# Performance work log

Measured on AMD Instinct MI355X. Metric: run time of the kernel, lower is better.

## Reference

```python
import jax, jax.numpy as jnp
import numpy as np

B, S, I, H, O = 256, 2048, 32, 128, 1


def setup_inputs() -> dict:
    key = jax.random.key(0)
    ks = jax.random.split(key, 9)
    sI = 1.0 / np.sqrt(I)
    sH = 1.0 / np.sqrt(H)
    sD = 1.0 / np.sqrt(H * S)
    return {
        "x": jax.random.normal(ks[0], (B, S, I), jnp.float32),
        "Wi": jax.random.normal(ks[1], (I, H), jnp.float32) * sI,
        "bi": jax.random.normal(ks[2], (H,), jnp.float32) * sI,
        "Wh": jax.random.normal(ks[3], (H, H), jnp.float32) * sH,
        "bh": jax.random.normal(ks[4], (H,), jnp.float32) * sH,
        "Wa": jax.random.normal(ks[5], (H, 1), jnp.float32) * sH,
        "ba": jax.random.normal(ks[6], (1,), jnp.float32) * sH,
        "Wd": jax.random.normal(ks[7], (H * S, O), jnp.float32) * sD,
        "bd": jax.random.normal(ks[8], (O,), jnp.float32) * sD,
        "resDepth": 4,
    }


def _branch_ids(seq_len: int, resDepth: int) -> np.ndarray:
    # Encodes the per-step branch of ResRNN_Cell.forward (static in i, resDepth):
    # 0: i==0 (set hstart, h0 stays zero)   1: i==lag-2 -> h0=tanh(hn+hstart)
    # 4: resDepth==1 -> h0=tanh(hn+h0)      2: i%resDepth==0 -> h0=tanh(hn+ht), ht=hn
    # 3: else -> h0=tanh(hn)
    br = np.full(seq_len, 3, dtype=np.int32)
    br[(np.arange(seq_len) % resDepth) == 0] = 2
    if resDepth == 1:
        br[:] = 4
    br[seq_len - 2] = 1
    br[0] = 0
    return br


def reference(x, Wi, bi, Wh, bh, Wa, ba, Wd, bd, resDepth):
    batch, seq_len, _ = x.shape
    hid = Wh.shape[0]
    br = _branch_ids(seq_len, int(resDepth))
    f0, f1, f2, f4 = (jnp.asarray(br == k) for k in (0, 1, 2, 4))
    xs = jnp.swapaxes(x, 0, 1)  # (S, B, I)
    z = jnp.zeros((batch, hid), x.dtype)

    def step(carry, inp):
        h0, ht, hstart = carry
        xt, g0, g1, g2, g4 = inp
        hn = xt @ Wi + bi + h0 @ Wh + bh  # (B, H)
        hstart = jnp.where(g0, hn, hstart)
        cand = jnp.where(g1, jnp.tanh(hn + hstart),
               jnp.where(g4, jnp.tanh(hn + h0),
               jnp.where(g2, jnp.tanh(hn + ht), jnp.tanh(hn))))
        h0n = jnp.where(g0, h0, cand)  # at i==0 h0 is NOT updated in the original
        htn = jnp.where(g2, hn, ht)
        return (h0n, htn, hstart), hn

    _, hiddens = jax.lax.scan(step, (z, z, z), (xs, f0, f1, f2, f4))
    # hiddens: (S, B, H) == torch.cat(outputs, 0)
    scores = hiddens @ Wa + ba  # (S, B, 1)
    # faithful to the original's .view((batchSize, -1)) on (S,B,1)-contiguous data
    att = jax.nn.softmax(scores.reshape(batch, seq_len), axis=-1)
    att = att.reshape(seq_len, batch, 1)
    weighted = hiddens * att  # (S, B, H)
    # faithful to .view(-1, hiddenNum * seq_len) on (S,B,H)-contiguous data
    flat = weighted.reshape(batch, seq_len * hid)
    return flat @ Wd + bd
```

## Files before the change

### kernel.cpp

```cpp
#include <hip/hip_runtime.h>
#include <math.h>

#define B_ 256
#define S_ 2048
#define I_ 32
#define H_ 128

__device__ __forceinline__ void sync_lds() {
    asm volatile("" ::: "memory");
    asm volatile("s_waitcnt lgkmcnt(0)" ::: "memory");
    __builtin_amdgcn_s_barrier();
    asm volatile("" ::: "memory");
}

__device__ __forceinline__ float fast_tanh(float z) {
    float e = __expf(2.0f * z);
    return 1.0f - 2.0f / (e + 1.0f);
}

template <int CTRL>
__device__ __forceinline__ float dppf(float v) {
    return __int_as_float(__builtin_amdgcn_update_dpp(
        0, __float_as_int(v), CTRL, 0xF, 0xF, false));
}

__device__ __forceinline__ float swz_xor16(float v) {
    return __int_as_float(__builtin_amdgcn_ds_swizzle(__float_as_int(v), 0x401F));
}
__device__ __forceinline__ float bperm_f(int addr_bytes, float v) {
    return __int_as_float(__builtin_amdgcn_ds_bpermute(addr_bytes, __float_as_int(v)));
}

#define MAC1(hval, idx)                              \
    a0 = fmaf(hval, WhR[(idx) * 2 + 0], a0);         \
    a1 = fmaf(hval, WhR[(idx) * 2 + 1], a1);
#define MAC4(hv, j)                                  \
    MAC1((hv).x, 4 * (j) + 0)                        \
    MAC1((hv).y, 4 * (j) + 1)                        \
    MAC1((hv).z, 4 * (j) + 2)                        \
    MAC1((hv).w, 4 * (j) + 3)

#define STEP_BODY(g, PH, XA, XB, CPH)                                         \
  {                                                                           \
    const int s_ = (g) * 8 + (PH);                                            \
    const float4* hsrc = (const float4*)&h0_lds[(PH) & 1][0];                 \
    float4 hv0 = hsrc[kg];                                                    \
    float4 hv1 = hsrc[kg + 8];                                                \
    float4 hv2 = hsrc[kg + 16];                                               \
    float4 hv3 = hsrc[kg + 24];                                               \
    if (s_ >= 1) {                \
      float r = uP;                                                           \
      r += dppf<0xB1>(r);                                                     \
      r += dppf<0x124>(r);                                                    \
      r += swz_xor16(r);                                                      \
      r += bperm_f(bp32, r);                                                  \
      if ((l & 0x3D) == 0)                                                    \
        ((float*)&pl_lds[(unsigned)(s_ - 1) & 3][w])[(l >> 1) & 1] = r;       \
    }                                                                         \
    if (w == 0 && s_ >= 2) {                \
      float2 pp = pl_lds[(unsigned)(s_ - 2) & 3][l & 7];                      \
      float px = pp.x, py = pp.y;                                             \
      px += dppf<0xB1>(px);  py += dppf<0xB1>(py);                            \
      px += dppf<0x4E>(px);  py += dppf<0x4E>(py);                            \
      px += dppf<0x124>(px); py += dppf<0x124>(py);                           \
      if (l == 0) part[((s_ - 2) << 8) + b] = make_float2(px, py);            \
    }                                                                         \
    float a0 = 0.f, a1 = 0.f;                                                 \
    MAC4(hv0, 0) MAC4(hv1, 1) MAC4(hv2, 2) MAC4(hv3, 3)                       \
    a0 += dppf<0xB1>(a0);                                                     \
    a1 += dppf<0xB1>(a1);                                                     \
    float t = kb0b ? a1 : a0;                                                 \
    float xwp = biasR;                                                        \
    xwp = fmaf((XA).x, WiC[0], xwp);                                          \
    xwp = fmaf((XA).y, WiC[1], xwp);                                          \
    xwp = fmaf((XA).z, WiC[2], xwp);                                          \
    xwp = fmaf((XA).w, WiC[3], xwp);                                          \
    xwp = fmaf((XB).x, WiC[4], xwp);                                          \
    xwp = fmaf((XB).y, WiC[5], xwp);                                          \
    xwp = fmaf((XB).z, WiC[6], xwp);                                          \
    xwp = fmaf((XB).w, WiC[7], xwp);                                          \
    t += xwp;                                \
    t += dppf<0x4E>(t);                                                       \
    t += dppf<0x128>(t);                                                      \
    float hn = t;                                                             \
    if (s_ < S_ - 2) {           \
      const float4* xr = (const float4*)(xgrp + ((PH) + 2) * I_);             \
      (XA) = xr[0]; (XB) = xr[1];                                             \
    }                                                                         \
    uP = hn * (CPH);                         \
    float h0n;                                                                \
    if (s_ == 0)            { hstartR = hn; h0n = 0.0f; }                     \
    else if (s_ == S_ - 2)  { h0n = fast_tanh(hn + hstartR); }                \
    else if (rd == 1)       { h0n = fast_tanh(hn + h0R); }                    \
    else if (cnt == 0)      { h0n = fast_tanh(hn + htR); htR = hn; }          \
    else                    { h0n = fast_tanh(hn); }                          \
    h0R = h0n;                                                                \
    if (wmask) h0_lds[((PH) + 1) & 1][hf] = h0n;                              \
    cnt = (cnt + 1 == rd) ? 0 : cnt + 1;                                      \
    sync_lds();                                                               \
  }

__global__ __launch_bounds__(512)
__attribute__((amdgpu_waves_per_eu(2, 2)))
void rnn_kernel(
    const float* __restrict__ x, const float* __restrict__ Wi,
    const float* __restrict__ bi, const float* __restrict__ Wh,
    const float* __restrict__ bh, const float* __restrict__ Wa,
    const float* __restrict__ Wd, const int* __restrict__ rdp,
    float2* __restrict__ part)
{
    const int b = blockIdx.x;
    const int t = threadIdx.x;
    const int w = t >> 6;
    const int l = t & 63;
    const int  kg    = (l & 3) | (((l >> 3) & 1) << 2);
    const int  hg    = ((l >> 2) & 1) | (((l >> 4) & 1) << 1)
                     | (((l >> 5) & 1) << 2);
    const int  hbase = 16 * w + 2 * hg;
    const int  hf    = hbase + (l & 1);
    const bool kb0b  = (l & 1);
    const bool wmask = ((l & 0xA) == 0);
    const int  i0x   = 8 * (((l >> 1) & 1) | (((l >> 3) & 1) << 1));
    const int  bp32  = (l ^ 32) << 2;

    __shared__ __align__(16) float h0_lds[2][H_];
    __shared__ __align__(8)  float2 pl_lds[4][8];

    const int rd = rdp[0];
    if (t < H_) h0_lds[0][t] = 0.0f;

    float WhR[32];
#pragma unroll
    for (int j = 0; j < 4; ++j)
#pragma unroll
        for (int c = 0; c < 4; ++c) {
            int k = 4 * kg + 32 * j + c;
            float2 wv = *(const float2*)(Wh + (size_t)k * H_ + hbase);
            WhR[(4 * j + c) * 2 + 0] = wv.x;
            WhR[(4 * j + c) * 2 + 1] = wv.y;
        }
    float WiC[8];
#pragma unroll
    for (int i = 0; i < 8; ++i) WiC[i] = Wi[(size_t)(i0x + i) * H_ + hf];
    const float biasR = wmask ? (bi[hf] + bh[hf]) : 0.0f;

    const bool clsq = (l >> 1) & 1;
    const float waC = Wa[hf];
    float cph[8];
#pragma unroll
    for (int K = 0; K < 8; ++K)
        cph[K] = clsq ? Wd[(K << 15) + (b << 7) + hf] : waC;

    const float* xgrp = x + (size_t)b * (S_ * I_) + i0x;
    float4 xA0 = ((const float4*)xgrp)[0];
    float4 xB0 = ((const float4*)xgrp)[1];
    float4 xA1 = ((const float4*)(xgrp + I_))[0];
    float4 xB1 = ((const float4*)(xgrp + I_))[1];

    sync_lds();

    float htR = 0.f, hstartR = 0.f, h0R = 0.f;
    float uP = 0.f;
    int cnt = 0;

    for (int g = 0; g < S_ / 8; ++g) {
        STEP_BODY(g, 0, xA0, xB0, cph[0])
        STEP_BODY(g, 1, xA1, xB1, cph[1])
        STEP_BODY(g, 2, xA0, xB0, cph[2])
        STEP_BODY(g, 3, xA1, xB1, cph[3])
        STEP_BODY(g, 4, xA0, xB0, cph[4])
        STEP_BODY(g, 5, xA1, xB1, cph[5])
        STEP_BODY(g, 6, xA0, xB0, cph[6])
        STEP_BODY(g, 7, xA1, xB1, cph[7])
        xgrp += 8 * I_;
    }

    {
        float r = uP;
        r += dppf<0xB1>(r);
        r += dppf<0x124>(r);
        r += swz_xor16(r);
        r += bperm_f(bp32, r);
        if ((l & 0x3D) == 0)
            ((float*)&pl_lds[3][w])[(l >> 1) & 1] = r;
    }
    sync_lds();
    if (w == 0) {
#pragma unroll
        for (int e = 0; e < 2; ++e) {
            float2 pp = pl_lds[2 + e][l & 7];
            float px = pp.x, py = pp.y;
            px += dppf<0xB1>(px);  py += dppf<0xB1>(py);
            px += dppf<0x4E>(px);  py += dppf<0x4E>(py);
            px += dppf<0x124>(px); py += dppf<0x124>(py);
            if (l == 0) part[((S_ - 2 + e) << 8) + b] = make_float2(px, py);
        }
    }
}

__global__ __launch_bounds__(256) void attn_kernel(
    const float2* __restrict__ part, const float* __restrict__ bd,
    float* __restrict__ out)
{
    const int r = blockIdx.x;
    const int t = threadIdx.x;
    float sc[8], dv[8];
    float mx = -1e30f;
#pragma unroll
    for (int u = 0; u < 8; ++u) {
        int f = (r << 11) + (u << 8) + t;
        float2 a = part[f];
        sc[u] = a.x;
        dv[u] = a.y;
        mx = fmaxf(mx, sc[u]);
    }
    __shared__ float redm[4], redz[4], redw[4];
#pragma unroll
    for (int off = 32; off > 0; off >>= 1) mx = fmaxf(mx, __shfl_xor(mx, off, 64));
    if ((t & 63) == 0) redm[t >> 6] = mx;
    __syncthreads();
    mx = fmaxf(fmaxf(redm[0], redm[1]), fmaxf(redm[2], redm[3]));
    float z = 0.f, wv = 0.f;
#pragma unroll
    for (int u = 0; u < 8; ++u) {
        float e = __expf(sc[u] - mx);
        z += e;
        wv += e * dv[u];
    }
#pragma unroll
    for (int off = 32; off > 0; off >>= 1) {
        z += __shfl_xor(z, off, 64);
        wv += __shfl_xor(wv, off, 64);
    }
    if ((t & 63) == 0) { redz[t >> 6] = z; redw[t >> 6] = wv; }
    __syncthreads();
    if (t == 0) {
        float Z = redz[0] + redz[1] + redz[2] + redz[3];
        float W = redw[0] + redw[1] + redw[2] + redw[3];
        out[r] = bd[0] + W / Z;
    }
}

extern "C" void kernel_launch(void* const* d_in, const int* in_sizes, int n_in,
                              void* d_out, int out_size, void* d_ws, size_t ws_size,
                              hipStream_t stream) {
    const float* x  = (const float*)d_in[0];
    const float* Wi = (const float*)d_in[1];
    const float* bi = (const float*)d_in[2];
    const float* Wh = (const float*)d_in[3];
    const float* bh = (const float*)d_in[4];
    const float* Wa = (const float*)d_in[5];
    const float* Wd = (const float*)d_in[7];
    const float* bd = (const float*)d_in[8];
    const int*  rdp = (const int*)d_in[9];

    float2* part = (float2*)d_ws;

    rnn_kernel<<<B_, 512, 0, stream>>>(x, Wi, bi, Wh, bh, Wa, Wd, rdp, part);
    attn_kernel<<<B_, 256, 0, stream>>>(part, bd, (float*)d_out);
}
```

Baseline: 1.035 ms.

## Halve RNN block to 4 waves with 4 hidden columns per lane

Each RNN block now runs with 256 threads instead of 512. Every lane holds four hidden columns of Wh and Wi as float4 registers, and the input projection is folded into the same accumulators before the cross-lane reduction. Using fewer waves per batch row should cut barrier cost and the cross-wave reduction work on each serial timestep. The trade-off is more FMAs per lane and a longer dependent chain in every step, and the per-lane register footprint roughly doubles.

```diff
diff --git a/kernel.cpp b/kernel.cpp
--- a/kernel.cpp
+++ b/kernel.cpp
@@ -31,61 +31,66 @@
     return __int_as_float(__builtin_amdgcn_ds_bpermute(addr_bytes, __float_as_int(v)));
 }
 
-#define MAC1(hval, idx)                              \
-    a0 = fmaf(hval, WhR[(idx) * 2 + 0], a0);         \
-    a1 = fmaf(hval, WhR[(idx) * 2 + 1], a1);
-#define MAC4(hv, j)                                  \
-    MAC1((hv).x, 4 * (j) + 0)                        \
-    MAC1((hv).y, 4 * (j) + 1)                        \
-    MAC1((hv).z, 4 * (j) + 2)                        \
-    MAC1((hv).w, 4 * (j) + 3)
-
-#define STEP_BODY(g, PH, XA, XB, CPH)                                         \
+#define MACC(hval, idx)                              \
+    a0 = fmaf(hval, WhR4[(idx)].x, a0);              \
+    a1 = fmaf(hval, WhR4[(idx)].y, a1);              \
+    a2 = fmaf(hval, WhR4[(idx)].z, a2);              \
+    a3 = fmaf(hval, WhR4[(idx)].w, a3);
+#define MACQ(hv, q)                                  \
+    MACC((hv).x, 4 * (q) + 0)                        \
+    MACC((hv).y, 4 * (q) + 1)                        \
+    MACC((hv).z, 4 * (q) + 2)                        \
+    MACC((hv).w, 4 * (q) + 3)
+
+#define STEP_BODY(g, PH, XS, CPH)                                             \
   {                                                                           \
     const int s_ = (g) * 8 + (PH);                                            \
     const float4* hsrc = (const float4*)&h0_lds[(PH) & 1][0];                 \
-    float4 hv0 = hsrc[kg];                                                    \
-    float4 hv1 = hsrc[kg + 8];                                                \
-    float4 hv2 = hsrc[kg + 16];                                               \
-    float4 hv3 = hsrc[kg + 24];                                               \
+    float4 hv0 = hsrc[kg3];                                                   \
+    float4 hv1 = hsrc[kg3 + 8];                                               \
+    float4 hv2 = hsrc[kg3 + 16];                                              \
+    float4 hv3 = hsrc[kg3 + 24];                                              \
     if (s_ >= 1) {                \
       float r = uP;                                                           \
       r += dppf<0xB1>(r);                                                     \
-      r += dppf<0x124>(r);                                                    \
+      r += dppf<0x4E>(r);                                                     \
+      r += dppf<0x141>(r);                                                    \
       r += swz_xor16(r);                                                      \
       r += bperm_f(bp32, r);                                                  \
-      if ((l & 0x3D) == 0)                                                    \
-        ((float*)&pl_lds[(unsigned)(s_ - 1) & 3][w])[(l >> 1) & 1] = r;       \
+      if ((l & 0x37) == 0)                                                    \
+        ((float*)&pl_lds[(unsigned)(s_ - 1) & 3][w])[(l >> 3) & 1] = r;       \
     }                                                                         \
     if (w == 0 && s_ >= 2) {                \
-      float2 pp = pl_lds[(unsigned)(s_ - 2) & 3][l & 7];                      \
+      float2 pp = pl_lds[(unsigned)(s_ - 2) & 3][l & 3];                      \
       float px = pp.x, py = pp.y;                                             \
       px += dppf<0xB1>(px);  py += dppf<0xB1>(py);                            \
       px += dppf<0x4E>(px);  py += dppf<0x4E>(py);                            \
-      px += dppf<0x124>(px); py += dppf<0x124>(py);                           \
       if (l == 0) part[((s_ - 2) << 8) + b] = make_float2(px, py);            \
     }                                                                         \
-    float a0 = 0.f, a1 = 0.f;                                                 \
-    MAC4(hv0, 0) MAC4(hv1, 1) MAC4(hv2, 2) MAC4(hv3, 3)                       \
-    a0 += dppf<0xB1>(a0);                                                     \
-    a1 += dppf<0xB1>(a1);                                                     \
-    float t = kb0b ? a1 : a0;                                                 \
-    float xwp = biasR;                                                        \
-    xwp = fmaf((XA).x, WiC[0], xwp);                                          \
-    xwp = fmaf((XA).y, WiC[1], xwp);                                          \
-    xwp = fmaf((XA).z, WiC[2], xwp);                                          \
-    xwp = fmaf((XA).w, WiC[3], xwp);                                          \
-    xwp = fmaf((XB).x, WiC[4], xwp);                                          \
-    xwp = fmaf((XB).y, WiC[5], xwp);                                          \
-    xwp = fmaf((XB).z, WiC[6], xwp);                                          \
-    xwp = fmaf((XB).w, WiC[7], xwp);                                          \
-    t += xwp;                                \
-    t += dppf<0x4E>(t);                                                       \
-    t += dppf<0x128>(t);                                                      \
-    float hn = t;                                                             \
+    float a0 = (XS).x * WiC4[0].x;                                            \
+    float a1 = (XS).x * WiC4[0].y;                                            \
+    float a2 = (XS).x * WiC4[0].z;                                            \
+    float a3 = (XS).x * WiC4[0].w;                                            \
+    a0 = fmaf((XS).y, WiC4[1].x, a0); a1 = fmaf((XS).y, WiC4[1].y, a1);       \
+    a2 = fmaf((XS).y, WiC4[1].z, a2); a3 = fmaf((XS).y, WiC4[1].w, a3);       \
+    a0 = fmaf((XS).z, WiC4[2].x, a0); a1 = fmaf((XS).z, WiC4[2].y, a1);       \
+    a2 = fmaf((XS).z, WiC4[2].z, a2); a3 = fmaf((XS).z, WiC4[2].w, a3);       \
+    a0 = fmaf((XS).w, WiC4[3].x, a0); a1 = fmaf((XS).w, WiC4[3].y, a1);       \
+    a2 = fmaf((XS).w, WiC4[3].z, a2); a3 = fmaf((XS).w, WiC4[3].w, a3);       \
+    MACQ(hv0, 0) MACQ(hv1, 1) MACQ(hv2, 2) MACQ(hv3, 3)                       \
+    float s0 = a0 + dppf<0xB1>(a0);                                           \
+    float s1 = a1 + dppf<0xB1>(a1);                                           \
+    float s2 = a2 + dppf<0xB1>(a2);                                           \
+    float s3 = a3 + dppf<0xB1>(a3);                                           \
+    float u0 = kb0 ? s1 : s0;                                                 \
+    float u1 = kb0 ? s3 : s2;                                                 \
+    u0 += dppf<0x4E>(u0);                                                     \
+    u1 += dppf<0x4E>(u1);                                                     \
+    float tt = kb1 ? u1 : u0;                                                 \
+    tt += dppf<0x128>(tt);                                                    \
+    float hn = tt + biasR;                                                    \
     if (s_ < S_ - 2) {           \
-      const float4* xr = (const float4*)(xgrp + ((PH) + 2) * I_);             \
-      (XA) = xr[0]; (XB) = xr[1];                                             \
+      (XS) = *(const float4*)(xgrp + ((PH) + 2) * I_);                        \
     }                                                                         \
     uP = hn * (CPH);                         \
     float h0n;                                                                \
@@ -100,8 +105,8 @@
     sync_lds();                                                               \
   }
 
-__global__ __launch_bounds__(512)
-__attribute__((amdgpu_waves_per_eu(2, 2)))
+__global__ __launch_bounds__(256)
+__attribute__((amdgpu_waves_per_eu(1, 1)))
 void rnn_kernel(
     const float* __restrict__ x, const float* __restrict__ Wi,
     const float* __restrict__ bi, const float* __restrict__ Wh,
@@ -113,38 +118,38 @@
     const int t = threadIdx.x;
     const int w = t >> 6;
     const int l = t & 63;
-    const int  kg    = (l & 3) | (((l >> 3) & 1) << 2);
+    const int  kg3   = (l & 3) | (((l >> 3) & 1) << 2);
     const int  hg    = ((l >> 2) & 1) | (((l >> 4) & 1) << 1)
                      | (((l >> 5) & 1) << 2);
-    const int  hbase = 16 * w + 2 * hg;
-    const int  hf    = hbase + (l & 1);
-    const bool kb0b  = (l & 1);
-    const bool wmask = ((l & 0xA) == 0);
-    const int  i0x   = 8 * (((l >> 1) & 1) | (((l >> 3) & 1) << 1));
-    const int  bp32  = (l ^ 32) << 2;
+    const int  hbase4 = 32 * w + 4 * hg;
+    const int  hf     = hbase4 + (l & 3);
+    const bool kb0    = (l & 1);
+    const bool kb1    = (l >> 1) & 1;
+    const bool wmask  = ((l & 8) == 0);
+    const int  i0x    = 4 * kg3;
+    const int  bp32   = (l ^ 32) << 2;
 
     __shared__ __align__(16) float h0_lds[2][H_];
-    __shared__ __align__(8)  float2 pl_lds[4][8];
+    __shared__ __align__(8)  float2 pl_lds[4][4];
 
     const int rd = rdp[0];
     if (t < H_) h0_lds[0][t] = 0.0f;
 
-    float WhR[32];
-#pragma unroll
-    for (int j = 0; j < 4; ++j)
+    float4 WhR4[16];
+#pragma unroll
+    for (int q = 0; q < 4; ++q)
 #pragma unroll
         for (int c = 0; c < 4; ++c) {
-            int k = 4 * kg + 32 * j + c;
-            float2 wv = *(const float2*)(Wh + (size_t)k * H_ + hbase);
-            WhR[(4 * j + c) * 2 + 0] = wv.x;
-            WhR[(4 * j + c) * 2 + 1] = wv.y;
+            int k = 4 * (kg3 + 8 * q) + c;
+            WhR4[q * 4 + c] = *(const float4*)(Wh + (size_t)k * H_ + hbase4);
         }
-    float WiC[8];
-#pragma unroll
-    for (int i = 0; i < 8; ++i) WiC[i] = Wi[(size_t)(i0x + i) * H_ + hf];
-    const float biasR = wmask ? (bi[hf] + bh[hf]) : 0.0f;
-
-    const bool clsq = (l >> 1) & 1;
+    float4 WiC4[4];
+#pragma unroll
+    for (int i = 0; i < 4; ++i)
+        WiC4[i] = *(const float4*)(Wi + (size_t)(i0x + i) * H_ + hbase4);
+    const float biasR = bi[hf] + bh[hf];
+
+    const bool clsq = (l >> 3) & 1;
     const float waC = Wa[hf];
     float cph[8];
 #pragma unroll
@@ -152,10 +157,8 @@
         cph[K] = clsq ? Wd[(K << 15) + (b << 7) + hf] : waC;
 
     const float* xgrp = x + (size_t)b * (S_ * I_) + i0x;
-    float4 xA0 = ((const float4*)xgrp)[0];
-    float4 xB0 = ((const float4*)xgrp)[1];
-    float4 xA1 = ((const float4*)(xgrp + I_))[0];
-    float4 xB1 = ((const float4*)(xgrp + I_))[1];
+    float4 xS0 = *(const float4*)xgrp;
+    float4 xS1 = *(const float4*)(xgrp + I_);
 
     sync_lds();
 
@@ -164,35 +167,35 @@
     int cnt = 0;
 
     for (int g = 0; g < S_ / 8; ++g) {
-        STEP_BODY(g, 0, xA0, xB0, cph[0])
-        STEP_BODY(g, 1, xA1, xB1, cph[1])
-        STEP_BODY(g, 2, xA0, xB0, cph[2])
-        STEP_BODY(g, 3, xA1, xB1, cph[3])
-        STEP_BODY(g, 4, xA0, xB0, cph[4])
-        STEP_BODY(g, 5, xA1, xB1, cph[5])
-        STEP_BODY(g, 6, xA0, xB0, cph[6])
-        STEP_BODY(g, 7, xA1, xB1, cph[7])
+        STEP_BODY(g, 0, xS0, cph[0])
+        STEP_BODY(g, 1, xS1, cph[1])
+        STEP_BODY(g, 2, xS0, cph[2])
+        STEP_BODY(g, 3, xS1, cph[3])
+        STEP_BODY(g, 4, xS0, cph[4])
+        STEP_BODY(g, 5, xS1, cph[5])
+        STEP_BODY(g, 6, xS0, cph[6])
+        STEP_BODY(g, 7, xS1, cph[7])
         xgrp += 8 * I_;
     }
 
     {
         float r = uP;
         r += dppf<0xB1>(r);
-        r += dppf<0x124>(r);
+        r += dppf<0x4E>(r);
+        r += dppf<0x141>(r);
         r += swz_xor16(r);
         r += bperm_f(bp32, r);
-        if ((l & 0x3D) == 0)
-            ((float*)&pl_lds[3][w])[(l >> 1) & 1] = r;
+        if ((l & 0x37) == 0)
+            ((float*)&pl_lds[3][w])[(l >> 3) & 1] = r;
     }
     sync_lds();
     if (w == 0) {
 #pragma unroll
         for (int e = 0; e < 2; ++e) {
-            float2 pp = pl_lds[2 + e][l & 7];
+            float2 pp = pl_lds[2 + e][l & 3];
             float px = pp.x, py = pp.y;
             px += dppf<0xB1>(px);  py += dppf<0xB1>(py);
             px += dppf<0x4E>(px);  py += dppf<0x4E>(py);
-            px += dppf<0x124>(px); py += dppf<0x124>(py);
             if (l == 0) part[((S_ - 2 + e) << 8) + b] = make_float2(px, py);
         }
     }
@@ -256,6 +259,6 @@
 
     float2* part = (float2*)d_ws;
 
-    rnn_kernel<<<B_, 512, 0, stream>>>(x, Wi, bi, Wh, bh, Wa, Wd, rdp, part);
+    rnn_kernel<<<B_, 256, 0, stream>>>(x, Wi, bi, Wh, bh, Wa, Wd, rdp, part);
     attn_kernel<<<B_, 256, 0, stream>>>(part, bd, (float*)d_out);
 }
```

Measured after the change: 1.079 ms. 1.04x slower.

## Peel first/last step groups, lighten per-step reductions and rotate combine across waves

Applied to the files above, without the earlier changes.

Peels the first and last 8-step groups so the middle loop runs a branch-light step with a select-based residual instead of the if-chain. The per-step attention/dense partial reduction drops the cross-half swizzle and bpermute, writing 32 partials per ring slot to LDS instead of 8. The final combine, which now does more DPP work plus a swizzle, rotates across waves by step phase instead of always running on wave 0. This shortens the serial critical path of each recurrent step at the cost of a larger LDS ring and more code.

```diff
diff --git a/kernel.cpp b/kernel.cpp
--- a/kernel.cpp
+++ b/kernel.cpp
@@ -26,9 +26,6 @@
 
 __device__ __forceinline__ float swz_xor16(float v) {
     return __int_as_float(__builtin_amdgcn_ds_swizzle(__float_as_int(v), 0x401F));
-}
-__device__ __forceinline__ float bperm_f(int addr_bytes, float v) {
-    return __int_as_float(__builtin_amdgcn_ds_bpermute(addr_bytes, __float_as_int(v)));
 }
 
 #define MAC1(hval, idx)                              \
@@ -40,36 +37,33 @@
     MAC1((hv).z, 4 * (j) + 2)                        \
     MAC1((hv).w, 4 * (j) + 3)
 
-#define STEP_BODY(g, PH, XA, XB, CPH)                                         \
-  {                                                                           \
-    const int s_ = (g) * 8 + (PH);                                            \
-    const float4* hsrc = (const float4*)&h0_lds[(PH) & 1][0];                 \
-    float4 hv0 = hsrc[kg];                                                    \
-    float4 hv1 = hsrc[kg + 8];                                                \
-    float4 hv2 = hsrc[kg + 16];                                               \
-    float4 hv3 = hsrc[kg + 24];                                               \
-    if (s_ >= 1) {                \
+#define UP_REDUCE(RING)                                                       \
+    {                                                                         \
       float r = uP;                                                           \
       r += dppf<0xB1>(r);                                                     \
       r += dppf<0x124>(r);                                                    \
-      r += swz_xor16(r);                                                      \
-      r += bperm_f(bp32, r);                                                  \
-      if ((l & 0x3D) == 0)                                                    \
-        ((float*)&pl_lds[(unsigned)(s_ - 1) & 3][w])[(l >> 1) & 1] = r;       \
-    }                                                                         \
-    if (w == 0 && s_ >= 2) {                \
-      float2 pp = pl_lds[(unsigned)(s_ - 2) & 3][l & 7];                      \
+      if ((l & 0xD) == 0)                                                     \
+        ((float*)&pl_lds[RING][(w << 2) | ((l >> 4) & 3)])[(l >> 1) & 1] = r; \
+    }
+
+#define PL_COMBINE(RING, SIDX)                                                \
+    {                                                                         \
+      float2 pp = pl_lds[RING][l & 31];                                       \
       float px = pp.x, py = pp.y;                                             \
       px += dppf<0xB1>(px);  py += dppf<0xB1>(py);                            \
       px += dppf<0x4E>(px);  py += dppf<0x4E>(py);                            \
-      px += dppf<0x124>(px); py += dppf<0x124>(py);                           \
-      if (l == 0) part[((s_ - 2) << 8) + b] = make_float2(px, py);            \
-    }                                                                         \
+      px += dppf<0x141>(px); py += dppf<0x141>(py);                           \
+      px += dppf<0x128>(px); py += dppf<0x128>(py);                           \
+      px += swz_xor16(px);   py += swz_xor16(py);                             \
+      if (l == 0) part[((SIDX) << 8) + b] = make_float2(px, py);              \
+    }
+
+#define MAT_CORE(XA, XB)                                                      \
     float a0 = 0.f, a1 = 0.f;                                                 \
     MAC4(hv0, 0) MAC4(hv1, 1) MAC4(hv2, 2) MAC4(hv3, 3)                       \
     a0 += dppf<0xB1>(a0);                                                     \
     a1 += dppf<0xB1>(a1);                                                     \
-    float t = kb0b ? a1 : a0;                                                 \
+    float tt = kb0b ? a1 : a0;                                                \
     float xwp = biasR;                                                        \
     xwp = fmaf((XA).x, WiC[0], xwp);                                          \
     xwp = fmaf((XA).y, WiC[1], xwp);                                          \
@@ -79,21 +73,59 @@
     xwp = fmaf((XB).y, WiC[5], xwp);                                          \
     xwp = fmaf((XB).z, WiC[6], xwp);                                          \
     xwp = fmaf((XB).w, WiC[7], xwp);                                          \
-    t += xwp;                                \
-    t += dppf<0x4E>(t);                                                       \
-    t += dppf<0x128>(t);                                                      \
-    float hn = t;                                                             \
-    if (s_ < S_ - 2) {           \
+    tt += xwp;                                                                \
+    tt += dppf<0x4E>(tt);                                                     \
+    tt += dppf<0x128>(tt);                                                    \
+    const float hn = tt;
+
+#define STEP_FULL(g, PH, XA, XB, CPH)                                         \
+  {                                                                           \
+    const int s_ = (g) * 8 + (PH);                                            \
+    const float4* hsrc = (const float4*)&h0_lds[(PH) & 1][0];                 \
+    float4 hv0 = hsrc[kg];                                                    \
+    float4 hv1 = hsrc[kg + 8];                                                \
+    float4 hv2 = hsrc[kg + 16];                                               \
+    float4 hv3 = hsrc[kg + 24];                                               \
+    if (s_ >= 1) UP_REDUCE(((PH) + 3) & 3)                                    \
+    if (w == (PH) && s_ >= 2) PL_COMBINE(((PH) + 2) & 3, s_ - 2)              \
+    MAT_CORE(XA, XB)                                                          \
+    if (s_ < S_ - 2) {                                                        \
       const float4* xr = (const float4*)(xgrp + ((PH) + 2) * I_);             \
       (XA) = xr[0]; (XB) = xr[1];                                             \
     }                                                                         \
-    uP = hn * (CPH);                         \
+    uP = hn * (CPH);                                                          \
     float h0n;                                                                \
     if (s_ == 0)            { hstartR = hn; h0n = 0.0f; }                     \
     else if (s_ == S_ - 2)  { h0n = fast_tanh(hn + hstartR); }                \
     else if (rd == 1)       { h0n = fast_tanh(hn + h0R); }                    \
     else if (cnt == 0)      { h0n = fast_tanh(hn + htR); htR = hn; }          \
     else                    { h0n = fast_tanh(hn); }                          \
+    h0R = h0n;                                                                \
+    if (wmask) h0_lds[((PH) + 1) & 1][hf] = h0n;                              \
+    cnt = (cnt + 1 == rd) ? 0 : cnt + 1;                                      \
+    sync_lds();                                                               \
+  }
+
+#define STEP_LEAN(g, PH, XA, XB, CPH)                                         \
+  {                                                                           \
+    const int s_ = (g) * 8 + (PH);                                            \
+    const float4* hsrc = (const float4*)&h0_lds[(PH) & 1][0];                 \
+    float4 hv0 = hsrc[kg];                                                    \
+    float4 hv1 = hsrc[kg + 8];                                                \
+    float4 hv2 = hsrc[kg + 16];                                               \
+    float4 hv3 = hsrc[kg + 24];                                               \
+    UP_REDUCE(((PH) + 3) & 3)                                                 \
+    if (w == (PH)) PL_COMBINE(((PH) + 2) & 3, s_ - 2)                         \
+    MAT_CORE(XA, XB)                                                          \
+    {                                                                         \
+      const float4* xr = (const float4*)(xgrp + ((PH) + 2) * I_);             \
+      (XA) = xr[0]; (XB) = xr[1];                                             \
+    }                                                                         \
+    uP = hn * (CPH);                                                          \
+    const bool c0 = (cnt == 0);                                               \
+    float resid = rd1 ? h0R : (c0 ? htR : 0.0f);                              \
+    float h0n = fast_tanh(hn + resid);                                        \
+    htR = (htup && c0) ? hn : htR;                                            \
     h0R = h0n;                                                                \
     if (wmask) h0_lds[((PH) + 1) & 1][hf] = h0n;                              \
     cnt = (cnt + 1 == rd) ? 0 : cnt + 1;                                      \
@@ -121,12 +153,13 @@
     const bool kb0b  = (l & 1);
     const bool wmask = ((l & 0xA) == 0);
     const int  i0x   = 8 * (((l >> 1) & 1) | (((l >> 3) & 1) << 1));
-    const int  bp32  = (l ^ 32) << 2;
 
     __shared__ __align__(16) float h0_lds[2][H_];
-    __shared__ __align__(8)  float2 pl_lds[4][8];
+    __shared__ __align__(8)  float2 pl_lds[4][32];
 
     const int rd = rdp[0];
+    const bool rd1  = (rd == 1);
+    const bool htup = !rd1;
     if (t < H_) h0_lds[0][t] = 0.0f;
 
     float WhR[32];
@@ -163,39 +196,43 @@
     float uP = 0.f;
     int cnt = 0;
 
-    for (int g = 0; g < S_ / 8; ++g) {
-        STEP_BODY(g, 0, xA0, xB0, cph[0])
-        STEP_BODY(g, 1, xA1, xB1, cph[1])
-        STEP_BODY(g, 2, xA0, xB0, cph[2])
-        STEP_BODY(g, 3, xA1, xB1, cph[3])
-        STEP_BODY(g, 4, xA0, xB0, cph[4])
-        STEP_BODY(g, 5, xA1, xB1, cph[5])
-        STEP_BODY(g, 6, xA0, xB0, cph[6])
-        STEP_BODY(g, 7, xA1, xB1, cph[7])
+    {
+        STEP_FULL(0, 0, xA0, xB0, cph[0])
+        STEP_FULL(0, 1, xA1, xB1, cph[1])
+        STEP_FULL(0, 2, xA0, xB0, cph[2])
+        STEP_FULL(0, 3, xA1, xB1, cph[3])
+        STEP_FULL(0, 4, xA0, xB0, cph[4])
+        STEP_FULL(0, 5, xA1, xB1, cph[5])
+        STEP_FULL(0, 6, xA0, xB0, cph[6])
+        STEP_FULL(0, 7, xA1, xB1, cph[7])
         xgrp += 8 * I_;
     }
-
+    for (int g = 1; g < 255; ++g) {
+        STEP_LEAN(g, 0, xA0, xB0, cph[0])
+        STEP_LEAN(g, 1, xA1, xB1, cph[1])
+        STEP_LEAN(g, 2, xA0, xB0, cph[2])
+        STEP_LEAN(g, 3, xA1, xB1, cph[3])
+        STEP_LEAN(g, 4, xA0, xB0, cph[4])
+        STEP_LEAN(g, 5, xA1, xB1, cph[5])
+        STEP_LEAN(g, 6, xA0, xB0, cph[6])
+        STEP_LEAN(g, 7, xA1, xB1, cph[7])
+        xgrp += 8 * I_;
+    }
     {
-        float r = uP;
-        r += dppf<0xB1>(r);
-        r += dppf<0x124>(r);
-        r += swz_xor16(r);
-        r += bperm_f(bp32, r);
-        if ((l & 0x3D) == 0)
-            ((float*)&pl_lds[3][w])[(l >> 1) & 1] = r;
-    }
+        STEP_FULL(255, 0, xA0, xB0, cph[0])
+        STEP_FULL(255, 1, xA1, xB1, cph[1])
+        STEP_FULL(255, 2, xA0, xB0, cph[2])
+        STEP_FULL(255, 3, xA1, xB1, cph[3])
+        STEP_FULL(255, 4, xA0, xB0, cph[4])
+        STEP_FULL(255, 5, xA1, xB1, cph[5])
+        STEP_FULL(255, 6, xA0, xB0, cph[6])
+        STEP_FULL(255, 7, xA1, xB1, cph[7])
+    }
+
+    UP_REDUCE(3)
     sync_lds();
-    if (w == 0) {
-#pragma unroll
-        for (int e = 0; e < 2; ++e) {
-            float2 pp = pl_lds[2 + e][l & 7];
-            float px = pp.x, py = pp.y;
-            px += dppf<0xB1>(px);  py += dppf<0xB1>(py);
-            px += dppf<0x4E>(px);  py += dppf<0x4E>(py);
-            px += dppf<0x124>(px); py += dppf<0x124>(py);
-            if (l == 0) part[((S_ - 2 + e) << 8) + b] = make_float2(px, py);
-        }
-    }
+    if (w == 0) PL_COMBINE(2, S_ - 2)
+    if (w == 1) PL_COMBINE(3, S_ - 1)
 }
 
 __global__ __launch_bounds__(256) void attn_kernel(
```

Result: faster. 929.4 us (-10.2%).
